# Kernel optimization log

Hardware: AMD Instinct MI355X
Metric: run time of the kernel (lower is better)

## Reference

```python
import jax, jax.numpy as jnp
from jax import lax
import numpy as np

B, T, D, H, C = 64, 512, 256, 1024, 128
ATT_SIG_W = 3.0


def _p(key, shape, scale=0.02):
    return (jax.random.normal(key, shape, dtype=jnp.float32) * scale)


def setup_inputs() -> dict:
    key = jax.random.key(0)
    ks = jax.random.split(key, 16)
    return {
        "x": jax.random.normal(ks[0], (B, T, D), dtype=jnp.float32),
        "i2h_w": _p(ks[1], (D, H)), "i2h_b": jnp.zeros((H,), jnp.float32),
        "h2h_w": _p(ks[2], (H, H)), "h2h_b": jnp.zeros((H,), jnp.float32),
        "fc_w": _p(ks[3], (H, C)), "fc_b": jnp.zeros((C,), jnp.float32),
        "att_wi_fwd": _p(ks[4], (D, 4 * H)), "att_wh_fwd": _p(ks[5], (H, 4 * H)),
        "att_b_fwd": jnp.zeros((4 * H,), jnp.float32),
        "att_wi_bwd": _p(ks[6], (D, 4 * H)), "att_wh_bwd": _p(ks[7], (H, 4 * H)),
        "att_b_bwd": jnp.zeros((4 * H,), jnp.float32),
        "att_fc_w": _p(ks[8], (2 * H, 1)), "att_fc_b": jnp.zeros((1,), jnp.float32),
    }


def _lstm(x_tbd, wi, wh, b):
    # x_tbd: [T,B,D]; precompute input projections as one batched GEMM
    pre = jnp.einsum('tbd,dh->tbh', x_tbd, wi) + b  # [T,B,4H]
    h0 = jnp.zeros((x_tbd.shape[1], wh.shape[0]), x_tbd.dtype)

    def step(carry, p):
        h, c = carry
        g = p + h @ wh
        i, f, gg, o = jnp.split(g, 4, axis=-1)
        c = jax.nn.sigmoid(f) * c + jax.nn.sigmoid(i) * jnp.tanh(gg)
        h = jax.nn.sigmoid(o) * jnp.tanh(c)
        return (h, c), h

    _, hs = lax.scan(step, (h0, h0), pre)
    return hs  # [T,B,H]


def reference(x, i2h_w, i2h_b, h2h_w, h2h_b, fc_w, fc_b,
              att_wi_fwd, att_wh_fwd, att_b_fwd,
              att_wi_bwd, att_wh_bwd, att_b_bwd,
              att_fc_w, att_fc_b):
    xt = jnp.transpose(x, (1, 0, 2))  # [T,B,D] (batch_first transpose)
    # AttentionNet: bidirectional LSTM -> linear -> steep sigmoid gate
    hf = _lstm(xt, att_wi_fwd, att_wh_fwd, att_b_fwd)
    hb = _lstm(xt[::-1], att_wi_bwd, att_wh_bwd, att_b_bwd)[::-1]
    hcat = jnp.concatenate([hf, hb], axis=-1)  # [T,B,2H]
    att_tb = jax.nn.sigmoid(ATT_SIG_W * (hcat @ att_fc_w + att_fc_b))[..., 0]  # [T,B]

    # TAGM recurrence: precompute i2h for all timesteps as one GEMM
    pre_i2h = jnp.einsum('tbd,dh->tbh', xt, i2h_w) + i2h_b  # [T,B,H]
    h0 = jnp.zeros((x.shape[0], h2h_w.shape[0]), x.dtype)

    def step(h, inp):
        p, a = inp  # p:[B,H], a:[B]
        cand = jax.nn.relu(p + h @ h2h_w + h2h_b)
        nh = a[:, None] * cand + (1.0 - a[:, None]) * h
        return nh, None

    h_last, _ = lax.scan(step, h0, (pre_i2h, att_tb))
    out = h_last @ fc_w + fc_b  # [B,C]
    attention = att_tb.T  # [B,T] to match original attention[:, i] layout
    return out, attention
```

## Files before the change

kernel.cpp:

```cpp
#include <hip/hip_runtime.h>
#include <hip/hip_bf16.h>
#include <cstdint>
#include <cstddef>

constexpr int BATCH = 64;
constexpr int SEQ   = 512;
constexpr int DIM   = 256;
constexpr int HID   = 1024;
constexpr int COUT  = 128;
constexpr int KTOT  = DIM + HID;
constexpr int NGATE = 4 * HID;
constexpr float ATT_SIG_W = 3.0f;

using bf16x8 = __attribute__((ext_vector_type(8))) __bf16;
using f32x4  = __attribute__((ext_vector_type(4))) float;
using u32x4  = __attribute__((ext_vector_type(4))) unsigned int;

__device__ __forceinline__ unsigned short f2bf(float f) {
    union { float f; unsigned u; } v; v.f = f;
    unsigned u = v.u;
    u += 0x7fffu + ((u >> 16) & 1u);
    return (unsigned short)(u >> 16);
}

__device__ __forceinline__ float sigm(float x) { return 1.f / (1.f + __expf(-x)); }

__device__ __forceinline__ void store_16B_wt(void* p, u32x4 v) {
    asm volatile("global_store_dwordx4 %0, %1, off sc0 sc1"
                 :: "v"(p), "v"(v) : "memory");
}

#define GLOAD_LDS_COHERENT(gptr, lptr)                                     \
    __builtin_amdgcn_global_load_lds(                                      \
        (const __attribute__((address_space(1))) void*)(gptr),             \
        (__attribute__((address_space(3))) void*)(lptr), 16, 0, 17)

__global__ void transpose_weights(const float* __restrict__ wi,
                                  const float* __restrict__ wh,
                                  unsigned short* __restrict__ out, int N) {
    __shared__ float tile[64][65];
    int ntiles = N >> 6;
    int kt = blockIdx.x / ntiles;
    int nt = blockIdx.x % ntiles;
    int k0 = kt << 6, n0 = nt << 6;
    int a = threadIdx.x & 63, g = threadIdx.x >> 6;
#pragma unroll
    for (int p = 0; p < 16; ++p) {
        int kr = p * 4 + g;
        int k = k0 + kr;
        const float* src = (k < DIM) ? (wi + (size_t)k * N) : (wh + (size_t)(k - DIM) * N);
        tile[kr][a] = src[n0 + a];
    }
    __syncthreads();
#pragma unroll
    for (int p = 0; p < 16; ++p) {
        int nr = p * 4 + g;
        out[(size_t)(n0 + nr) * KTOT + (k0 + a)] = f2bf(tile[a][nr]);
    }
}

__global__ void transpose_x(const float* __restrict__ x, unsigned short* __restrict__ xt) {
    size_t idx = (size_t)blockIdx.x * blockDim.x + threadIdx.x;
    if (idx >= (size_t)SEQ * BATCH * DIM) return;
    int d = idx % DIM;
    size_t r = idx / DIM;
    int b = r % BATCH;
    int t = r / BATCH;
    xt[idx] = f2bf(x[((size_t)b * SEQ + t) * DIM + d]);
}

__global__ void pack_lstm(const unsigned short* __restrict__ WT,
                          unsigned short* __restrict__ out) {
    int cg = blockIdx.x >> 1, kh = blockIdx.x & 1;
    size_t base = (size_t)blockIdx.x * 20480;
#pragma unroll
    for (int j = 0; j < 80; ++j) {
        int idx = threadIdx.x * 80 + j;
        int frag = idx >> 9;
        int rem = idx & 511;
        int lane = rem >> 3, e = rem & 7;
        int nt = frag / 20, ksl = frag % 20;
        int p = nt * 16 + (lane & 15);
        int origcol = (p >> 3) * 1024 + cg * 8 + (p & 7);
        int k = kh * 640 + ksl * 32 + ((lane >> 4) & 3) * 8 + e;
        out[base + idx] = WT[(size_t)origcol * KTOT + k];
    }
}

__global__ void pack_tagm(const unsigned short* __restrict__ WT,
                          unsigned short* __restrict__ out) {
    int cg = blockIdx.x >> 2, kq = blockIdx.x & 3;
    size_t base = (size_t)blockIdx.x * 5120;
#pragma unroll
    for (int j = 0; j < 20; ++j) {
        int idx = threadIdx.x * 20 + j;
        int ksl = idx >> 9;
        int rem = idx & 511;
        int lane = rem >> 3, e = rem & 7;
        int origcol = cg * 16 + (lane & 15);
        int k = kq * 320 + ksl * 32 + ((lane >> 4) & 3) * 8 + e;
        out[base + idx] = WT[(size_t)origcol * KTOT + k];
    }
}

__device__ __forceinline__ void flag_light(unsigned* flags, int base, int cnt,
                                           int myidx, unsigned epoch) {
    asm volatile("s_waitcnt vmcnt(0)" ::: "memory");
    __syncthreads();
    if (threadIdx.x == 0)
        __hip_atomic_store(flags + myidx, epoch, __ATOMIC_RELAXED, __HIP_MEMORY_SCOPE_AGENT);
    if (threadIdx.x < 64) {
        for (;;) {
            bool ok = true;
            for (int j = (int)threadIdx.x; j < cnt; j += 64)
                ok &= (__hip_atomic_load(flags + base + j, __ATOMIC_RELAXED,
                                         __HIP_MEMORY_SCOPE_AGENT) >= epoch);
            if (__all(ok)) break;
            __builtin_amdgcn_s_sleep(1);
        }
    }
    __syncthreads();
}

__device__ __forceinline__ void flag_barrier(unsigned* flags, int base, int cnt,
                                             int myidx, unsigned epoch) {
    __syncthreads();
    if (threadIdx.x == 0) {
        __builtin_amdgcn_fence(__ATOMIC_RELEASE, "agent");
        __hip_atomic_store(flags + myidx, epoch, __ATOMIC_RELAXED, __HIP_MEMORY_SCOPE_AGENT);
    }
    if (threadIdx.x < 64) {
        for (;;) {
            bool ok = true;
            for (int j = (int)threadIdx.x; j < cnt; j += 64)
                ok &= (__hip_atomic_load(flags + base + j, __ATOMIC_RELAXED,
                                         __HIP_MEMORY_SCOPE_AGENT) >= epoch);
            if (__all(ok)) break;
            __builtin_amdgcn_s_sleep(1);
        }
        if (threadIdx.x == 0)
            __builtin_amdgcn_fence(__ATOMIC_ACQUIRE, "agent");
    }
    __syncthreads();
}

__global__ __launch_bounds__(256)
void tagm_fused(const unsigned short* __restrict__ xt,
                const unsigned short* __restrict__ Wfp,
                const unsigned short* __restrict__ Wbp,
                const unsigned short* __restrict__ Wtp,
                const float* __restrict__ bias_f, const float* __restrict__ bias_b,
                const float* __restrict__ attw, const float* __restrict__ att_fc_b,
                const float* __restrict__ i2h_b, const float* __restrict__ h2h_b,
                const float* __restrict__ fc_w, const float* __restrict__ fc_b,
                unsigned short* __restrict__ h_lstm,
                unsigned short* __restrict__ h_tagm,
                float* __restrict__ h_f32,
                float* __restrict__ att_part,
                unsigned* __restrict__ flags,
                float* __restrict__ out) {
    extern __shared__ char smem[];
    char* dumpbase = smem + 65536;
    float* auxf = (float*)(smem + 65536 + 8192);
    unsigned short* hscr = (unsigned short*)(smem + 65536 + 8192 + 4096);

    int tid = threadIdx.x;
    int wave = tid >> 6, lane = tid & 63;
    int bid = blockIdx.x;
    int dir = bid & 1, rh = (bid >> 1) & 1, cg = bid >> 2;
    int nc = wave >> 1, kh = wave & 1;
    int q = lane >> 4, c15 = lane & 15;
    int hc = lane & 7;

    bf16x8 wreg[40];
    {
        const unsigned short* wp = (dir ? Wbp : Wfp)
                                   + (size_t)((cg * 2 + nc) * 2 + kh) * 20480;
#pragma unroll
        for (int f = 0; f < 40; ++f)
            wreg[f] = *(const bf16x8*)(wp + f * 512 + lane * 8);
    }
    int colE = cg * 16 + nc * 8 + hc;
    const float* bias = dir ? bias_b : bias_f;
    float b_ii = bias[colE], b_ff = bias[HID + colE];
    float b_gg = bias[2 * HID + colE], b_oo = bias[3 * HID + colE];
    float attw_l = attw[dir * HID + colE];

    for (int i = tid; i < 512; i += 256) auxf[i] = 0.f;

    flag_light(flags, 256, 256, 256 + bid, 1u);

    for (int t = 0; t < SEQ; ++t) {
        int tx = dir ? (SEQ - 1 - t) : t;
        const unsigned short* xrow = xt + (size_t)tx * BATCH * DIM;
        bf16x8 xa[16];
        if (kh == 0) {
#pragma unroll
            for (int ksl = 0; ksl < 8; ++ksl)
#pragma unroll
                for (int mt = 0; mt < 2; ++mt) {
                    int row = rh * 32 + mt * 16 + c15;
                    xa[ksl * 2 + mt] = *(const bf16x8*)(xrow + row * DIM + ksl * 32 + q * 8);
                }
        }
        if (t > 0) {
            for (;;) {
                bool ok = true;
                if (lane < 16)
                    ok = (__hip_atomic_load(flags + dir * 128 + rh * 64 + wave * 16 + lane,
                                            __ATOMIC_RELAXED,
                                            __HIP_MEMORY_SCOPE_AGENT) >= (unsigned)t);
                if (__all(ok)) break;
                __builtin_amdgcn_s_sleep(1);
            }
        }
        __builtin_amdgcn_sched_barrier(0);
        {
            const char* hsrc = (const char*)h_lstm
                               + (size_t)((dir * 2 + (t & 1)) * 2 + rh) * 65536;
            char* lbase = smem + (size_t)wave * 16384 + (size_t)lane * 16;
#pragma unroll
            for (int i = 0; i < 16; ++i) {
                int s = wave * 1024 + i * 64 + lane;
                GLOAD_LDS_COHERENT(hsrc + (size_t)s * 16, lbase + (size_t)i * 1024);
            }
        }
        __syncthreads();

        f32x4 acc[2][2] = {};
#pragma unroll
        for (int ksl = 0; ksl < 20; ++ksl) {
#pragma unroll
            for (int mt = 0; mt < 2; ++mt) {
                bf16x8 a;
                if (kh == 0 && ksl < 8) {
                    a = xa[ksl * 2 + mt];
                } else {
                    int kcol = kh * 640 + ksl * 32 + q * 8 - 256;
                    a = *(const bf16x8*)(smem + (size_t)(kcol >> 4) * 1024
                                         + (size_t)((kcol >> 3) & 1) * 512
                                         + (size_t)(mt * 16 + c15) * 16);
                }
                acc[mt][0] = __builtin_amdgcn_mfma_f32_16x16x32_bf16(a, wreg[ksl],      acc[mt][0], 0, 0, 0);
                acc[mt][1] = __builtin_amdgcn_mfma_f32_16x16x32_bf16(a, wreg[20 + ksl], acc[mt][1], 0, 0, 0);
            }
        }
        if (kh == 1) {
            float* dp = (float*)(dumpbase + nc * 4096);
#pragma unroll
            for (int mt = 0; mt < 2; ++mt)
#pragma unroll
                for (int nt = 0; nt < 2; ++nt)
                    *(f32x4*)(dp + ((mt * 2 + nt) * 64 + lane) * 4) = acc[mt][nt];
        }
        __syncthreads();
        if (kh == 0) {
            const float* dp = (const float*)(dumpbase + nc * 4096);
            bool low = (lane & 8) == 0;
#pragma unroll
            for (int mt = 0; mt < 2; ++mt) {
                f32x4 g0 = acc[mt][0] + *(const f32x4*)(dp + ((mt * 2 + 0) * 64 + lane) * 4);
                f32x4 g1 = acc[mt][1] + *(const f32x4*)(dp + ((mt * 2 + 1) * 64 + lane) * 4);
                f32x4 av4;
#pragma unroll
                for (int r = 0; r < 4; ++r) {
                    float fo0 = __shfl(g0[r], lane ^ 8);
                    float fo1 = __shfl(g1[r], lane ^ 8);
                    int rl = mt * 16 + q * 4 + r;
                    float si = sigm(g0[r] + b_ii);
                    float sf = sigm(fo0 + b_ff);
                    float tg = tanhf(g1[r] + b_gg);
                    float so = sigm(fo1 + b_oo);
                    float cprev = auxf[rl * 16 + nc * 8 + hc];
                    float cn = sf * cprev + si * tg;
                    float hn = so * tanhf(cn);
                    float av = low ? hn * attw_l : 0.f;
                    av += __shfl_xor(av, 1); av += __shfl_xor(av, 2); av += __shfl_xor(av, 4);
                    av4[r] = av;
                    if (low) {
                        auxf[rl * 16 + nc * 8 + hc] = cn;
                        hscr[nc * 256 + rl * 8 + hc] = f2bf(hn);
                    }
                }
                if (c15 == 0)
                    *(f32x4*)(att_part + (size_t)(bid * 2 + nc) * 16384
                              + (size_t)tx * 32 + (mt * 16 + q * 4)) = av4;
            }
        }
        __syncthreads();
        if (tid < 64) {
            u32x4 v = *(const u32x4*)(hscr + tid * 8);
            store_16B_wt((char*)h_lstm
                         + (size_t)((dir * 2 + ((t + 1) & 1)) * 2 + rh) * 65536
                         + (size_t)(cg * 64 + tid) * 16, v);
            asm volatile("s_waitcnt vmcnt(0)" ::: "memory");
            if (tid == 0)
                __hip_atomic_store(flags + dir * 128 + rh * 64 + cg, (unsigned)(t + 1),
                                   __ATOMIC_RELAXED, __HIP_MEMORY_SCOPE_AGENT);
        }
    }

    flag_barrier(flags, 256, 256, 256 + bid, 2u);
    {
        int i = tid & 127, half = tid >> 7;
        int item = bid * 128 + i;
        int tt = item >> 6, grow = item & 63;
        int rl = grow & 31, rh2 = grow >> 5;
        float s = 0.f;
        const float* p = att_part + (size_t)((half + rh2 * 2) * 2) * 16384
                         + (size_t)tt * 32 + rl;
        for (int cgi = 0; cgi < 64; ++cgi) {
            size_t off = (size_t)cgi * 8 * 16384;
            s += p[off] + p[off + 16384];
        }
        float* red = (float*)dumpbase;
        if (half) red[i] = s;
        __syncthreads();
        if (!half)
            out[BATCH * COUT + grow * SEQ + tt] = sigm(ATT_SIG_W * (s + red[i] + att_fc_b[0]));
    }
    flag_barrier(flags, 256, 256, 256 + bid, 3u);

    int rq = bid & 3, cgT = bid >> 2;
    int kq = wave;
    bf16x8 wt[10];
    {
        const unsigned short* wp = Wtp + (size_t)(cgT * 4 + kq) * 5120;
#pragma unroll
        for (int f = 0; f < 10; ++f)
            wt[f] = *(const bf16x8*)(wp + f * 512 + lane * 8);
    }
    int colT = cgT * 16 + c15;
    float bbT = i2h_b[colT] + h2h_b[colT];
    for (int i = tid; i < 256; i += 256) auxf[i] = 0.f;
    __syncthreads();
    const float* attd = out + BATCH * COUT;

    for (int t = 0; t < SEQ; ++t) {
        bf16x8 xa[8];
        if (kq == 0) {
            const unsigned short* xrow = xt + (size_t)t * BATCH * DIM;
#pragma unroll
            for (int ksl = 0; ksl < 8; ++ksl) {
                int row = rq * 16 + c15;
                xa[ksl] = *(const bf16x8*)(xrow + row * DIM + ksl * 32 + q * 8);
            }
        }
        if (t > 0) {
            for (;;) {
                bool ok = true;
                if (lane < 16)
                    ok = (__hip_atomic_load(flags + 512 + rq * 64 + wave * 16 + lane,
                                            __ATOMIC_RELAXED,
                                            __HIP_MEMORY_SCOPE_AGENT) >= (unsigned)t);
                if (__all(ok)) break;
                __builtin_amdgcn_s_sleep(1);
            }
        }
        __builtin_amdgcn_sched_barrier(0);
        {
            const char* hsrc = (const char*)h_tagm + (size_t)((t & 1) * 4 + rq) * 32768;
            char* lbase = smem + (size_t)wave * 8192 + (size_t)lane * 16;
#pragma unroll
            for (int i = 0; i < 8; ++i) {
                int s = wave * 512 + i * 64 + lane;
                GLOAD_LDS_COHERENT(hsrc + (size_t)s * 16, lbase + (size_t)i * 1024);
            }
        }
        __syncthreads();
        f32x4 acc = {};
#pragma unroll
        for (int ksl = 0; ksl < 10; ++ksl) {
            bf16x8 a;
            if (kq == 0 && ksl < 8) {
                a = xa[ksl];
            } else {
                int kcol = kq * 320 + ksl * 32 + q * 8 - 256;
                a = *(const bf16x8*)(smem + (size_t)(kcol >> 3) * 256
                                     + (size_t)c15 * 16);
            }
            acc = __builtin_amdgcn_mfma_f32_16x16x32_bf16(a, wt[ksl], acc, 0, 0, 0);
        }
        if (kq)
            *(f32x4*)(dumpbase + (kq - 1) * 1024 + lane * 16) = acc;
        __syncthreads();
        if (kq == 0) {
            f32x4 g = acc + *(const f32x4*)(dumpbase + lane * 16)
                          + *(const f32x4*)(dumpbase + 1024 + lane * 16)
                          + *(const f32x4*)(dumpbase + 2048 + lane * 16);
#pragma unroll
            for (int r = 0; r < 4; ++r) {
                int rl = q * 4 + r;
                float cand = g[r] + bbT;
                cand = cand > 0.f ? cand : 0.f;
                float a = attd[(rq * 16 + rl) * SEQ + t];
                float hold = auxf[rl * 16 + c15];
                float hn = a * cand + (1.f - a) * hold;
                auxf[rl * 16 + c15] = hn;
                hscr[(c15 >> 3) * 128 + rl * 8 + (c15 & 7)] = f2bf(hn);
            }
        }
        __syncthreads();
        if (tid < 32) {
            u32x4 v = *(const u32x4*)(hscr + tid * 8);
            store_16B_wt((char*)h_tagm + (size_t)((((t + 1) & 1)) * 4 + rq) * 32768
                         + (size_t)(cgT * 32 + tid) * 16, v);
            asm volatile("s_waitcnt vmcnt(0)" ::: "memory");
            if (tid == 0)
                __hip_atomic_store(flags + 512 + rq * 64 + cgT, (unsigned)(t + 1),
                                   __ATOMIC_RELAXED, __HIP_MEMORY_SCOPE_AGENT);
        }
    }

    for (int i = tid; i < 256; i += 256) {
        int rl = i >> 4, cl = i & 15;
        h_f32[(size_t)(rq * 16 + rl) * HID + cgT * 16 + cl] = auxf[i];
    }
    flag_barrier(flags, 768, 256, 768 + bid, 1u);
    if (bid >= 64) return;

    {
        float* fcp = (float*)dumpbase;
        int c = tid & 127, half = tid >> 7;
        const float* hrow = h_f32 + (size_t)bid * HID;
        float s = 0.f;
        for (int k = half * 512; k < half * 512 + 512; ++k)
            s += hrow[k] * fc_w[(size_t)k * COUT + c];
        fcp[half * 128 + c] = s;
        __syncthreads();
        if (tid < 128)
            out[bid * COUT + tid] = fcp[tid] + fcp[128 + tid] + fc_b[tid];
    }
}

extern "C" void kernel_launch(void* const* d_in, const int* in_sizes, int n_in,
                              void* d_out, int out_size, void* d_ws, size_t ws_size,
                              hipStream_t stream) {
    const float* x          = (const float*)d_in[0];
    const float* i2h_w      = (const float*)d_in[1];
    const float* i2h_b      = (const float*)d_in[2];
    const float* h2h_w      = (const float*)d_in[3];
    const float* h2h_b      = (const float*)d_in[4];
    const float* fc_w       = (const float*)d_in[5];
    const float* fc_b       = (const float*)d_in[6];
    const float* att_wi_fwd = (const float*)d_in[7];
    const float* att_wh_fwd = (const float*)d_in[8];
    const float* att_b_fwd  = (const float*)d_in[9];
    const float* att_wi_bwd = (const float*)d_in[10];
    const float* att_wh_bwd = (const float*)d_in[11];
    const float* att_b_bwd  = (const float*)d_in[12];
    const float* att_fc_w   = (const float*)d_in[13];
    const float* att_fc_b   = (const float*)d_in[14];
    float* out = (float*)d_out;

    char* ws = (char*)d_ws;
    unsigned short* WfT = (unsigned short*)(ws + 0);
    unsigned short* WbT = (unsigned short*)(ws + 10485760);
    unsigned short* WtT = (unsigned short*)(ws + 20971520);
    unsigned short* Wfp = (unsigned short*)(ws + 23592960);
    unsigned short* Wbp = (unsigned short*)(ws + 34078720);
    unsigned short* Wtp = (unsigned short*)(ws + 17829888);
    unsigned short* xtb    = (unsigned short*)(ws + 0);
    unsigned short* h_lstm = (unsigned short*)(ws + 16777216);
    unsigned short* h_tagm = (unsigned short*)(ws + 17301504);
    float*          h_f32  = (float*)(ws + 17563648);
    unsigned*       flags  = (unsigned*)(ws + 17825792);
    float*          att_part = (float*)(ws + 23592960);

    transpose_weights<<<20 * (NGATE / 64), 256, 0, stream>>>(att_wi_fwd, att_wh_fwd, WfT, NGATE);
    transpose_weights<<<20 * (NGATE / 64), 256, 0, stream>>>(att_wi_bwd, att_wh_bwd, WbT, NGATE);
    transpose_weights<<<20 * (HID / 64), 256, 0, stream>>>(i2h_w, h2h_w, WtT, HID);
    pack_lstm<<<256, 256, 0, stream>>>(WfT, Wfp);
    pack_lstm<<<256, 256, 0, stream>>>(WbT, Wbp);
    pack_tagm<<<256, 256, 0, stream>>>(WtT, Wtp);
    transpose_x<<<(SEQ * BATCH * DIM + 255) / 256, 256, 0, stream>>>(x, xtb);
    (void)hipMemsetAsync(ws + 16777216, 0, 17829888 - 16777216, stream);

    static const int SMEM_BYTES = 98304;
    (void)hipFuncSetAttribute(reinterpret_cast<const void*>(tagm_fused),
                              hipFuncAttributeMaxDynamicSharedMemorySize, SMEM_BYTES);
    tagm_fused<<<256, 256, SMEM_BYTES, stream>>>(
        xtb, Wfp, Wbp, Wtp, att_b_fwd, att_b_bwd, att_fc_w, att_fc_b,
        i2h_b, h2h_b, fc_w, fc_b, h_lstm, h_tagm, h_f32, att_part, flags, out);
}
```

Measured before the change: 6.219 ms.

## Overlap input-projection MFMAs with h loads and split gate epilogue across waves

In both the bidirectional LSTM and TAGM recurrent steps, the MFMAs on the register-resident x operand now run before the barrier that waits for the h vector to land in LDS. This hides part of the global-to-LDS load latency on the serial critical path. The cross-wave reduction is also changed so that every wave writes one partial tile, reads the others, and computes part of the gate or candidate epilogue, rather than leaving one wave group to do all of it. The trade-off is extra LDS traffic and more index math in exchange for a shorter per-timestep dependent chain.

```diff
diff --git a/kernel.cpp b/kernel.cpp
--- a/kernel.cpp
+++ b/kernel.cpp
@@ -225,67 +225,89 @@
                 GLOAD_LDS_COHERENT(hsrc + (size_t)s * 16, lbase + (size_t)i * 1024);
             }
         }
-        __syncthreads();
-
         f32x4 acc[2][2] = {};
-#pragma unroll
-        for (int ksl = 0; ksl < 20; ++ksl) {
-#pragma unroll
-            for (int mt = 0; mt < 2; ++mt) {
-                bf16x8 a;
-                if (kh == 0 && ksl < 8) {
-                    a = xa[ksl * 2 + mt];
-                } else {
-                    int kcol = kh * 640 + ksl * 32 + q * 8 - 256;
-                    a = *(const bf16x8*)(smem + (size_t)(kcol >> 4) * 1024
-                                         + (size_t)((kcol >> 3) & 1) * 512
-                                         + (size_t)(mt * 16 + c15) * 16);
+        if (kh == 0) {
+#pragma unroll
+            for (int ksl = 0; ksl < 8; ++ksl)
+#pragma unroll
+                for (int mt = 0; mt < 2; ++mt) {
+                    acc[mt][0] = __builtin_amdgcn_mfma_f32_16x16x32_bf16(xa[ksl * 2 + mt], wreg[ksl],      acc[mt][0], 0, 0, 0);
+                    acc[mt][1] = __builtin_amdgcn_mfma_f32_16x16x32_bf16(xa[ksl * 2 + mt], wreg[20 + ksl], acc[mt][1], 0, 0, 0);
                 }
-                acc[mt][0] = __builtin_amdgcn_mfma_f32_16x16x32_bf16(a, wreg[ksl],      acc[mt][0], 0, 0, 0);
-                acc[mt][1] = __builtin_amdgcn_mfma_f32_16x16x32_bf16(a, wreg[20 + ksl], acc[mt][1], 0, 0, 0);
-            }
-        }
-        if (kh == 1) {
-            float* dp = (float*)(dumpbase + nc * 4096);
-#pragma unroll
-            for (int mt = 0; mt < 2; ++mt)
-#pragma unroll
-                for (int nt = 0; nt < 2; ++nt)
-                    *(f32x4*)(dp + ((mt * 2 + nt) * 64 + lane) * 4) = acc[mt][nt];
-        }
-        __syncthreads();
+        }
+        __syncthreads();
+
         if (kh == 0) {
-            const float* dp = (const float*)(dumpbase + nc * 4096);
+#pragma unroll
+            for (int ksl = 8; ksl < 20; ++ksl)
+#pragma unroll
+                for (int mt = 0; mt < 2; ++mt) {
+                    int kcol = ksl * 32 + q * 8 - 256;
+                    bf16x8 a = *(const bf16x8*)(smem + (size_t)(kcol >> 4) * 1024
+                                                + (size_t)((kcol >> 3) & 1) * 512
+                                                + (size_t)(mt * 16 + c15) * 16);
+                    acc[mt][0] = __builtin_amdgcn_mfma_f32_16x16x32_bf16(a, wreg[ksl],      acc[mt][0], 0, 0, 0);
+                    acc[mt][1] = __builtin_amdgcn_mfma_f32_16x16x32_bf16(a, wreg[20 + ksl], acc[mt][1], 0, 0, 0);
+                }
+        } else {
+#pragma unroll
+            for (int ksl = 0; ksl < 20; ++ksl)
+#pragma unroll
+                for (int mt = 0; mt < 2; ++mt) {
+                    int kcol = 384 + ksl * 32 + q * 8;
+                    bf16x8 a = *(const bf16x8*)(smem + (size_t)(kcol >> 4) * 1024
+                                                + (size_t)((kcol >> 3) & 1) * 512
+                                                + (size_t)(mt * 16 + c15) * 16);
+                    acc[mt][0] = __builtin_amdgcn_mfma_f32_16x16x32_bf16(a, wreg[ksl],      acc[mt][0], 0, 0, 0);
+                    acc[mt][1] = __builtin_amdgcn_mfma_f32_16x16x32_bf16(a, wreg[20 + ksl], acc[mt][1], 0, 0, 0);
+                }
+        }
+        {
+            float* dp = (float*)(dumpbase + (nc * 2 + kh) * 2048);
+            if (kh == 0) {
+                *(f32x4*)(dp + (0 * 64 + lane) * 4) = acc[1][0];
+                *(f32x4*)(dp + (1 * 64 + lane) * 4) = acc[1][1];
+            } else {
+                *(f32x4*)(dp + (0 * 64 + lane) * 4) = acc[0][0];
+                *(f32x4*)(dp + (1 * 64 + lane) * 4) = acc[0][1];
+            }
+        }
+        __syncthreads();
+        {
+            const float* dq = (const float*)(dumpbase + (nc * 2 + (1 - kh)) * 2048);
+            f32x4 g0, g1;
+            if (kh == 0) {
+                g0 = acc[0][0] + *(const f32x4*)(dq + (0 * 64 + lane) * 4);
+                g1 = acc[0][1] + *(const f32x4*)(dq + (1 * 64 + lane) * 4);
+            } else {
+                g0 = acc[1][0] + *(const f32x4*)(dq + (0 * 64 + lane) * 4);
+                g1 = acc[1][1] + *(const f32x4*)(dq + (1 * 64 + lane) * 4);
+            }
             bool low = (lane & 8) == 0;
-#pragma unroll
-            for (int mt = 0; mt < 2; ++mt) {
-                f32x4 g0 = acc[mt][0] + *(const f32x4*)(dp + ((mt * 2 + 0) * 64 + lane) * 4);
-                f32x4 g1 = acc[mt][1] + *(const f32x4*)(dp + ((mt * 2 + 1) * 64 + lane) * 4);
-                f32x4 av4;
-#pragma unroll
-                for (int r = 0; r < 4; ++r) {
-                    float fo0 = __shfl(g0[r], lane ^ 8);
-                    float fo1 = __shfl(g1[r], lane ^ 8);
-                    int rl = mt * 16 + q * 4 + r;
-                    float si = sigm(g0[r] + b_ii);
-                    float sf = sigm(fo0 + b_ff);
-                    float tg = tanhf(g1[r] + b_gg);
-                    float so = sigm(fo1 + b_oo);
-                    float cprev = auxf[rl * 16 + nc * 8 + hc];
-                    float cn = sf * cprev + si * tg;
-                    float hn = so * tanhf(cn);
-                    float av = low ? hn * attw_l : 0.f;
-                    av += __shfl_xor(av, 1); av += __shfl_xor(av, 2); av += __shfl_xor(av, 4);
-                    av4[r] = av;
-                    if (low) {
-                        auxf[rl * 16 + nc * 8 + hc] = cn;
-                        hscr[nc * 256 + rl * 8 + hc] = f2bf(hn);
-                    }
+            f32x4 av4;
+#pragma unroll
+            for (int r = 0; r < 4; ++r) {
+                float fo0 = __shfl(g0[r], lane ^ 8);
+                float fo1 = __shfl(g1[r], lane ^ 8);
+                int rl = kh * 16 + q * 4 + r;
+                float si = sigm(g0[r] + b_ii);
+                float sf = sigm(fo0 + b_ff);
+                float tg = tanhf(g1[r] + b_gg);
+                float so = sigm(fo1 + b_oo);
+                float cprev = auxf[rl * 16 + nc * 8 + hc];
+                float cn = sf * cprev + si * tg;
+                float hn = so * tanhf(cn);
+                float av = low ? hn * attw_l : 0.f;
+                av += __shfl_xor(av, 1); av += __shfl_xor(av, 2); av += __shfl_xor(av, 4);
+                av4[r] = av;
+                if (low) {
+                    auxf[rl * 16 + nc * 8 + hc] = cn;
+                    hscr[nc * 256 + rl * 8 + hc] = f2bf(hn);
                 }
-                if (c15 == 0)
-                    *(f32x4*)(att_part + (size_t)(bid * 2 + nc) * 16384
-                              + (size_t)tx * 32 + (mt * 16 + q * 4)) = av4;
-            }
+            }
+            if (c15 == 0)
+                *(f32x4*)(att_part + (size_t)(bid * 2 + nc) * 16384
+                          + (size_t)tx * 32 + (kh * 16 + q * 4)) = av4;
         }
         __syncthreads();
         if (tid < 64) {
@@ -367,38 +389,45 @@
                 GLOAD_LDS_COHERENT(hsrc + (size_t)s * 16, lbase + (size_t)i * 1024);
             }
         }
-        __syncthreads();
         f32x4 acc = {};
-#pragma unroll
-        for (int ksl = 0; ksl < 10; ++ksl) {
-            bf16x8 a;
-            if (kq == 0 && ksl < 8) {
-                a = xa[ksl];
-            } else {
+        if (kq == 0) {
+#pragma unroll
+            for (int ksl = 0; ksl < 8; ++ksl)
+                acc = __builtin_amdgcn_mfma_f32_16x16x32_bf16(xa[ksl], wt[ksl], acc, 0, 0, 0);
+        }
+        __syncthreads();
+        if (kq == 0) {
+#pragma unroll
+            for (int ksl = 8; ksl < 10; ++ksl) {
+                int kcol = ksl * 32 + q * 8 - 256;
+                bf16x8 a = *(const bf16x8*)(smem + (size_t)(kcol >> 3) * 256
+                                            + (size_t)c15 * 16);
+                acc = __builtin_amdgcn_mfma_f32_16x16x32_bf16(a, wt[ksl], acc, 0, 0, 0);
+            }
+        } else {
+#pragma unroll
+            for (int ksl = 0; ksl < 10; ++ksl) {
                 int kcol = kq * 320 + ksl * 32 + q * 8 - 256;
-                a = *(const bf16x8*)(smem + (size_t)(kcol >> 3) * 256
-                                     + (size_t)c15 * 16);
-            }
-            acc = __builtin_amdgcn_mfma_f32_16x16x32_bf16(a, wt[ksl], acc, 0, 0, 0);
-        }
-        if (kq)
-            *(f32x4*)(dumpbase + (kq - 1) * 1024 + lane * 16) = acc;
-        __syncthreads();
-        if (kq == 0) {
-            f32x4 g = acc + *(const f32x4*)(dumpbase + lane * 16)
-                          + *(const f32x4*)(dumpbase + 1024 + lane * 16)
-                          + *(const f32x4*)(dumpbase + 2048 + lane * 16);
-#pragma unroll
-            for (int r = 0; r < 4; ++r) {
-                int rl = q * 4 + r;
-                float cand = g[r] + bbT;
-                cand = cand > 0.f ? cand : 0.f;
-                float a = attd[(rq * 16 + rl) * SEQ + t];
-                float hold = auxf[rl * 16 + c15];
-                float hn = a * cand + (1.f - a) * hold;
-                auxf[rl * 16 + c15] = hn;
-                hscr[(c15 >> 3) * 128 + rl * 8 + (c15 & 7)] = f2bf(hn);
-            }
+                bf16x8 a = *(const bf16x8*)(smem + (size_t)(kcol >> 3) * 256
+                                            + (size_t)c15 * 16);
+                acc = __builtin_amdgcn_mfma_f32_16x16x32_bf16(a, wt[ksl], acc, 0, 0, 0);
+            }
+        }
+        *(f32x4*)(dumpbase + kq * 1024 + lane * 16) = acc;
+        __syncthreads();
+        {
+            int rr = lane >> 4;
+            int col = c15;
+            int row = kq * 4 + rr;
+            const float* db = (const float*)dumpbase;
+            int e = (kq * 16 + col) * 4 + rr;
+            float g = db[e] + db[256 + e] + db[512 + e] + db[768 + e] + bbT;
+            float cand = g > 0.f ? g : 0.f;
+            float a = attd[(rq * 16 + row) * SEQ + t];
+            float hold = auxf[row * 16 + col];
+            float hn = a * cand + (1.f - a) * hold;
+            auxf[row * 16 + col] = hn;
+            hscr[(col >> 3) * 128 + row * 8 + (col & 7)] = f2bf(hn);
         }
         __syncthreads();
         if (tid < 32) {
```

Result: faster. 6.051 ms (-2.7%).
